# Kernel tuning notes

Hardware: AMD Instinct MI355X
Metric: run time of the kernel (lower is better)

## Reference

```python
import jax, jax.numpy as jnp
import numpy as np

B, KPLUS1, D = 64, 513, 1024

def setup_inputs() -> dict:
    key = jax.random.key(0)
    k1, k2, k3 = jax.random.split(key, 3)
    x = jax.random.normal(k1, (B, KPLUS1, D), dtype=jnp.float32)
    # glorot-style scaled init for faithfulness in magnitude
    dense_weights = jax.random.normal(k2, (2 * D, D), dtype=jnp.float32) * (1.0 / np.sqrt(2 * D))
    dot_bias = jax.random.normal(k3, (D, 1), dtype=jnp.float32) * (1.0 / np.sqrt(D))
    return {"x": x, "dense_weights": dense_weights, "dot_bias": dot_bias}

def reference(x, dense_weights, dot_bias):
    # x: [B, K+1, D]; x[:,0] = sentence encoding u, x[:,1:] = knowledge z_t
    u = x[:, 0, :]            # [B, D]
    z = x[:, 1:, :]           # [B, K, D]
    d = z.shape[-1]
    # concat(z_t, u) @ W1 == z @ W1[:D] + u @ W1[D:], broadcast over K
    # (mathematically identical to the tile+concat+matmul in the original)
    w_z = dense_weights[:d, :]   # [D, D]
    w_u = dense_weights[d:, :]   # [D, D]
    m = jnp.tanh(jnp.einsum('bkd,de->bke', z, w_z)
                 + jnp.einsum('bd,de->be', u, w_u)[:, None, :])  # [B, K, D]
    q = jnp.einsum('bke,e->bk', m, dot_bias[:, 0])               # [B, K]
    return jax.nn.softmax(q, axis=-1)                            # [B, K]
```

## Files before the change

### kernel.cpp

```cpp
#include <hip/hip_runtime.h>
#include <hip/hip_bf16.h>


typedef __attribute__((ext_vector_type(8))) short short8;
typedef __attribute__((ext_vector_type(8))) _Float16 half8;
typedef __attribute__((ext_vector_type(4))) float f32x4;
typedef unsigned short ushort_t;

typedef const __attribute__((address_space(1))) void gvoid_t;
typedef __attribute__((address_space(3))) void lvoid_t;

__device__ __forceinline__ ushort_t f2bf(float f) {
    unsigned u = __float_as_uint(f);
    unsigned r = u + 0x7FFFu + ((u >> 16) & 1u);
    return (ushort_t)(r >> 16);
}
__device__ __forceinline__ float bf2f(ushort_t h) {
    return __uint_as_float(((unsigned)h) << 16);
}
__device__ __forceinline__ float tanh_fast(float x) {
    float e = __expf(2.f * x);
    return 1.f - 2.f / (e + 1.f);
}

__global__ __launch_bounds__(256) void k_prep_z16(const float* __restrict__ x,
                                                  _Float16* __restrict__ z_h) {
    const int N8 = 32768 * 128;
    const int stride = 2048 * 256;
    for (int u = blockIdx.x * 256 + threadIdx.x; u < N8; u += stride) {
        const int m = u >> 7;
        const int c = (u & 127) * 8;
        const int b = m >> 9, k = m & 511;
        const float* src = x + ((size_t)(b * 513 + 1 + k) << 10) + c;
        const float4 v0 = *(const float4*)src;
        const float4 v1 = *(const float4*)(src + 4);
        half8 hv;
        hv[0] = (_Float16)v0.x; hv[1] = (_Float16)v0.y;
        hv[2] = (_Float16)v0.z; hv[3] = (_Float16)v0.w;
        hv[4] = (_Float16)v1.x; hv[5] = (_Float16)v1.y;
        hv[6] = (_Float16)v1.z; hv[7] = (_Float16)v1.w;
        *(half8*)(z_h + (size_t)m * 1024 + c) = hv;
    }
}

__global__ void k_prep_w16(const float* __restrict__ w,
                           _Float16* __restrict__ wzt) {
    __shared__ _Float16 th[64][66];
    const int k0 = blockIdx.x * 64;
    const int n0 = blockIdx.y * 64;
    const int t = threadIdx.x;
    const int lr = t >> 6;
    const int lc = t & 63;
#pragma unroll
    for (int r = 0; r < 16; ++r) {
        int kk = r * 4 + lr;
        th[kk][lc] = (_Float16)w[(size_t)(k0 + kk) * 1024 + n0 + lc];
    }
    __syncthreads();
#pragma unroll
    for (int r = 0; r < 16; ++r) {
        int nn = r * 4 + lr;
        wzt[(size_t)(n0 + nn) * 1024 + k0 + lc] = th[lc][nn];
    }
}

__global__ void k_hu(const float* __restrict__ x,
                     const float* __restrict__ w,
                     float* __restrict__ hu) {
    __shared__ float us[1024];
    const int b = blockIdx.y;
    const int e = blockIdx.x * 256 + threadIdx.x;
    for (int i = threadIdx.x; i < 1024; i += 256)
        us[i] = x[(size_t)b * 513 * 1024 + i];
    __syncthreads();
    const float* wu = w + (size_t)1024 * 1024;
    float acc = 0.f;
#pragma unroll 8
    for (int d = 0; d < 1024; ++d)
        acc = fmaf(us[d], wu[(size_t)d * 1024 + e], acc);
    hu[b * 1024 + e] = acc;
}

__global__ __launch_bounds__(256, 2) void k_gemm12(
        const _Float16* __restrict__ z_h,
        const _Float16* __restrict__ wzt,
        const float* __restrict__ hu,
        const float* __restrict__ bias,
        float* __restrict__ qp) {
    __shared__ __align__(16) _Float16 lds[3 * 12288];
    __shared__ float qred[2][2][128];

    const int t = threadIdx.x;
    const int mtile = blockIdx.x;
    const int ntile = blockIdx.y;
    const int wid = t >> 6;
    const int l = t & 63;
    const int wm = wid >> 1;
    const int wn = wid & 1;
    const int lr = l & 15;
    const int g = l >> 4;

    char* ldsb = (char*)lds;

    const int swz = (g ^ ((lr >> 1) & 3)) * 16;
    const int aOffRd = (wm * 128 + lr) * 64 + swz;
    const int bOffRd = (wn * 64 + lr) * 64 + swz;

    const int srow = t >> 2;
    const int schunk = ((t & 3) ^ ((t >> 3) & 3)) * 8;
    size_t aSrc[4], bSrc[2];
#pragma unroll
    for (int s = 0; s < 4; ++s)
        aSrc[s] = (size_t)(mtile * 256 + s * 64 + srow) * 1024 + schunk;
#pragma unroll
    for (int s = 0; s < 2; ++s)
        bSrc[s] = (size_t)(ntile * 128 + s * 64 + srow) * 1024 + schunk;

#define STAGE(kt, SLOT)                                                      \
    {   const int _kc = (kt) * 32;                                           \
        char* _d = ldsb + (SLOT) * 24576;                                    \
        _Pragma("unroll")                                                    \
        for (int s = 0; s < 4; ++s)                                          \
            __builtin_amdgcn_global_load_lds((gvoid_t*)(z_h + aSrc[s] + _kc),\
                (lvoid_t*)(_d + s * 4096 + t * 16), 16, 0, 0);               \
        _Pragma("unroll")                                                    \
        for (int s = 0; s < 2; ++s)                                          \
            __builtin_amdgcn_global_load_lds((gvoid_t*)(wzt + bSrc[s] + _kc),\
                (lvoid_t*)(_d + 16384 + s * 4096 + t * 16), 16, 0, 0); }

#define KBODY(T, SLOT, DOSTAGE, VMSTR)                                       \
    {   char* _sb = ldsb + (SLOT) * 24576;                                   \
        half8 afr[8], bfr[4];                                                \
        _Pragma("unroll")                                                    \
        for (int ni = 0; ni < 4; ++ni)                                       \
            bfr[ni] = *(const half8*)(_sb + 16384 + bOffRd + ni * 1024);     \
        _Pragma("unroll")                                                    \
        for (int mi = 0; mi < 8; ++mi)                                       \
            afr[mi] = *(const half8*)(_sb + aOffRd + mi * 1024);             \
        if (DOSTAGE) { STAGE((T) + 2, ((SLOT) + 2) % 3); }                   \
        asm volatile("s_waitcnt lgkmcnt(0)" ::: "memory");                   \
        __builtin_amdgcn_sched_barrier(0);                                   \
        __builtin_amdgcn_s_setprio(1);                                       \
        _Pragma("unroll")                                                    \
        for (int mi = 0; mi < 8; ++mi)                                       \
            _Pragma("unroll")                                                \
            for (int ni = 0; ni < 4; ++ni)                                   \
                acc[mi][ni] = __builtin_amdgcn_mfma_f32_16x16x32_f16(        \
                    afr[mi], bfr[ni], acc[mi][ni], 0, 0, 0);                 \
        __builtin_amdgcn_s_setprio(0);                                       \
        asm volatile(VMSTR ::: "memory");                                    \
        __builtin_amdgcn_sched_barrier(0);                                   \
        __builtin_amdgcn_s_barrier(); }

    f32x4 acc[8][4] = {};

    STAGE(0, 0); STAGE(1, 1);
    asm volatile("s_waitcnt vmcnt(6)" ::: "memory");
    __builtin_amdgcn_sched_barrier(0);
    __builtin_amdgcn_s_barrier();

#pragma unroll 1
    for (int i = 0; i < 10; ++i) {
        const int T = i * 3;
        KBODY(T + 0, 0, true, "s_waitcnt vmcnt(6)");
        KBODY(T + 1, 1, true, "s_waitcnt vmcnt(6)");
        KBODY(T + 2, 2, true, "s_waitcnt vmcnt(6)");
    }
    KBODY(30, 0, false, "s_waitcnt vmcnt(0)");
    KBODY(31, 1, false, "s_nop 0");
#undef KBODY
#undef STAGE

    const int lg = l >> 4;
    const int bb = mtile >> 1;
    float hu4[4], bias4[4];
#pragma unroll
    for (int ni = 0; ni < 4; ++ni) {
        int e = ntile * 128 + wn * 64 + ni * 16 + lr;
        hu4[ni] = hu[bb * 1024 + e];
        bias4[ni] = bias[e];
    }
#pragma unroll
    for (int mi = 0; mi < 8; ++mi) {
#pragma unroll
        for (int j = 0; j < 4; ++j) {
            float v = 0.f;
#pragma unroll
            for (int ni = 0; ni < 4; ++ni)
                v += tanh_fast(acc[mi][ni][j] + hu4[ni]) * bias4[ni];
            v += __shfl_xor(v, 1);
            v += __shfl_xor(v, 2);
            v += __shfl_xor(v, 4);
            v += __shfl_xor(v, 8);
            if (lr == 0)
                qred[wm][wn][mi * 16 + lg * 4 + j] = v;
        }
    }
    __syncthreads();
    if (t < 256) {
        float q = qred[t >> 7][0][t & 127] + qred[t >> 7][1][t & 127];
        qp[(size_t)ntile * 32768 + mtile * 256 + t] = q;
    }
}

__global__ void k_prep_w(const float* __restrict__ w,
                         ushort_t* __restrict__ wzt_hi,
                         ushort_t* __restrict__ wzt_lo) {
    __shared__ ushort_t th[64][66];
    __shared__ ushort_t tl[64][66];
    const int k0 = blockIdx.x * 64;
    const int n0 = blockIdx.y * 64;
    const int t = threadIdx.x;
    const int lr = t >> 6;
    const int lc = t & 63;
#pragma unroll
    for (int r = 0; r < 16; ++r) {
        int kk = r * 4 + lr;
        float f = w[(size_t)(k0 + kk) * 1024 + n0 + lc];
        ushort_t hi = f2bf(f);
        ushort_t lo = f2bf(f - bf2f(hi));
        th[kk][lc] = hi;
        tl[kk][lc] = lo;
    }
    __syncthreads();
#pragma unroll
    for (int r = 0; r < 16; ++r) {
        int nn = r * 4 + lr;
        wzt_hi[(size_t)(n0 + nn) * 1024 + k0 + lc] = th[lc][nn];
        wzt_lo[(size_t)(n0 + nn) * 1024 + k0 + lc] = tl[lc][nn];
    }
}

__global__ __launch_bounds__(256) void k_gemm(
        const float* __restrict__ x,
        const ushort_t* __restrict__ wzt_hi,
        const ushort_t* __restrict__ wzt_lo,
        const float* __restrict__ hu,
        const float* __restrict__ bias,
        float* __restrict__ qp) {
    __shared__ ushort_t As_hi[128][40];
    __shared__ ushort_t As_lo[128][40];
    __shared__ ushort_t Bs_hi[128][40];
    __shared__ ushort_t Bs_lo[128][40];
    __shared__ float qred[2][2][64];

    const int t = threadIdx.x;
    const int mtile = blockIdx.x;
    const int ntile = blockIdx.y;
    const int wid = t >> 6;
    const int l = t & 63;
    const int wm = wid >> 1;
    const int wn = wid & 1;

    f32x4 acc[4][4] = {};

    const int arow = t >> 3;
    const int acol = (t & 7) * 4;
    size_t abase[4];
#pragma unroll
    for (int it = 0; it < 4; ++it) {
        int m = mtile * 128 + arow + it * 32;
        int bb = m >> 9;
        int kk = m & 511;
        abase[it] = ((size_t)(bb * 513 + 1 + kk)) * 1024 + acol;
    }
    const int brow = t >> 2;
    const int bcol = (t & 3) * 8;
    const size_t bbase = (size_t)(ntile * 128 + brow) * 1024 + bcol;

    for (int k0 = 0; k0 < 1024; k0 += 32) {
#pragma unroll
        for (int it = 0; it < 4; ++it) {
            const float4 v = *(const float4*)(x + abase[it] + k0);
            ushort4 hv, lv;
            hv.x = f2bf(v.x); lv.x = f2bf(v.x - bf2f(hv.x));
            hv.y = f2bf(v.y); lv.y = f2bf(v.y - bf2f(hv.y));
            hv.z = f2bf(v.z); lv.z = f2bf(v.z - bf2f(hv.z));
            hv.w = f2bf(v.w); lv.w = f2bf(v.w - bf2f(hv.w));
            const int row = arow + it * 32;
            *(ushort4*)&As_hi[row][acol] = hv;
            *(ushort4*)&As_lo[row][acol] = lv;
        }
#pragma unroll
        for (int it = 0; it < 2; ++it) {
            const int row = brow + it * 64;
            const uint4 vh = *(const uint4*)(wzt_hi + bbase + (size_t)it * 64 * 1024 + k0);
            const uint4 vl = *(const uint4*)(wzt_lo + bbase + (size_t)it * 64 * 1024 + k0);
            *(uint4*)&Bs_hi[row][bcol] = vh;
            *(uint4*)&Bs_lo[row][bcol] = vl;
        }
        __syncthreads();

        const int lr = l & 15;
        const int lk = (l >> 4) * 8;
        short8 ah[4], al[4], bh[4], bl[4];
#pragma unroll
        for (int i = 0; i < 4; ++i) {
            ah[i] = *(const short8*)&As_hi[wm * 64 + i * 16 + lr][lk];
            al[i] = *(const short8*)&As_lo[wm * 64 + i * 16 + lr][lk];
            bh[i] = *(const short8*)&Bs_hi[wn * 64 + i * 16 + lr][lk];
            bl[i] = *(const short8*)&Bs_lo[wn * 64 + i * 16 + lr][lk];
        }
#pragma unroll
        for (int mi = 0; mi < 4; ++mi)
#pragma unroll
            for (int ni = 0; ni < 4; ++ni) {
                acc[mi][ni] = __builtin_amdgcn_mfma_f32_16x16x32_bf16(ah[mi], bh[ni], acc[mi][ni], 0, 0, 0);
                acc[mi][ni] = __builtin_amdgcn_mfma_f32_16x16x32_bf16(ah[mi], bl[ni], acc[mi][ni], 0, 0, 0);
                acc[mi][ni] = __builtin_amdgcn_mfma_f32_16x16x32_bf16(al[mi], bh[ni], acc[mi][ni], 0, 0, 0);
            }
        __syncthreads();
    }

    const int lr = l & 15;
    const int lg = l >> 4;
    const int bbatch = mtile >> 2;
    float hu4[4], bias4[4];
#pragma unroll
    for (int ni = 0; ni < 4; ++ni) {
        int e = ntile * 128 + wn * 64 + ni * 16 + lr;
        hu4[ni] = hu[bbatch * 1024 + e];
        bias4[ni] = bias[e];
    }
#pragma unroll
    for (int mi = 0; mi < 4; ++mi) {
#pragma unroll
        for (int j = 0; j < 4; ++j) {
            float v = 0.f;
#pragma unroll
            for (int ni = 0; ni < 4; ++ni)
                v += tanhf(acc[mi][ni][j] + hu4[ni]) * bias4[ni];
            v += __shfl_xor(v, 1);
            v += __shfl_xor(v, 2);
            v += __shfl_xor(v, 4);
            v += __shfl_xor(v, 8);
            if (lr == 0)
                qred[wm][wn][mi * 16 + lg * 4 + j] = v;
        }
    }
    __syncthreads();
    if (t < 128) {
        const int wmr = t >> 6;
        const int rr = t & 63;
        float qv = qred[wmr][0][rr] + qred[wmr][1][rr];
        qp[(size_t)ntile * 32768 + mtile * 128 + t] = qv;
    }
}

__global__ void k_softmax(const float* __restrict__ qp, float* __restrict__ out,
                          int nt) {
    const int b = blockIdx.x;
    const int k = threadIdx.x;
    float q = 0.f;
    for (int i = 0; i < nt; ++i)
        q += qp[(size_t)i * 32768 + b * 512 + k];

    __shared__ float redm[8];
    __shared__ float reds[8];
    const int wid = k >> 6;

    float m = q;
#pragma unroll
    for (int off = 32; off >= 1; off >>= 1)
        m = fmaxf(m, __shfl_xor(m, off));
    if ((k & 63) == 0) redm[wid] = m;
    __syncthreads();
    m = redm[0];
#pragma unroll
    for (int i = 1; i < 8; ++i) m = fmaxf(m, redm[i]);

    float p = expf(q - m);
    float s = p;
#pragma unroll
    for (int off = 32; off >= 1; off >>= 1)
        s += __shfl_xor(s, off);
    if ((k & 63) == 0) reds[wid] = s;
    __syncthreads();
    s = 0.f;
#pragma unroll
    for (int i = 0; i < 8; ++i) s += reds[i];

    out[b * 512 + k] = p / s;
}

extern "C" void kernel_launch(void* const* d_in, const int* in_sizes, int n_in,
                              void* d_out, int out_size, void* d_ws, size_t ws_size,
                              hipStream_t stream) {
    const float* x    = (const float*)d_in[0];
    const float* w    = (const float*)d_in[1];
    const float* bias = (const float*)d_in[2];
    float* out = (float*)d_out;

    char* ws = (char*)d_ws;
    const size_t ZN = (size_t)32768 * 1024;

    const size_t need = ZN * sizeof(_Float16)
                      + (size_t)1024 * 1024 * sizeof(_Float16)
                      + (size_t)64 * 1024 * sizeof(float)
                      + (size_t)8 * 32768 * sizeof(float);

    if (ws_size >= need) {
        _Float16* z_h = (_Float16*)ws;
        _Float16* wzt = z_h + ZN;
        float*    hu  = (float*)(wzt + (size_t)1024 * 1024);
        float*    qp  = hu + (size_t)64 * 1024;

        k_prep_z16<<<2048, 256, 0, stream>>>(x, z_h);
        k_prep_w16<<<dim3(16, 16), 256, 0, stream>>>(w, wzt);
        k_hu<<<dim3(4, 64), 256, 0, stream>>>(x, w, hu);
        k_gemm12<<<dim3(128, 8), 256, 0, stream>>>(z_h, wzt, hu, bias, qp);
        k_softmax<<<64, 512, 0, stream>>>(qp, out, 8);
    } else {
        ushort_t* wzt_hi = (ushort_t*)ws;
        ushort_t* wzt_lo = wzt_hi + (size_t)1024 * 1024;
        float* hu = (float*)(ws + (size_t)4 * 1024 * 1024);
        float* qp = hu + (size_t)64 * 1024;

        k_prep_w<<<dim3(16, 16), 256, 0, stream>>>(w, wzt_hi, wzt_lo);
        k_hu<<<dim3(4, 64), 256, 0, stream>>>(x, w, hu);
        k_gemm<<<dim3(256, 8), 256, 0, stream>>>(x, wzt_hi, wzt_lo, hu, bias, qp);
        k_softmax<<<64, 512, 0, stream>>>(qp, out, 8);
    }
}
```

Baseline: 185.2 us.

## Enlarge GEMM block tile to 256x256 with eight waves per block

The fused GEMM+tanh+dot kernel now uses 512-thread blocks, each computing a 256x256 output tile instead of 256x128. The grid is halved along N and the softmax reduces over four partial-q slices instead of eight. The goal is to cut global and L2 traffic per FLOP by reusing each A tile across twice as many columns. In exchange LDS use rises to 96KB per block and occupancy drops to roughly one block per CU.

```diff
diff --git a/kernel.cpp b/kernel.cpp
--- a/kernel.cpp
+++ b/kernel.cpp
@@ -81,22 +81,22 @@
     hu[b * 1024 + e] = acc;
 }
 
-__global__ __launch_bounds__(256, 2) void k_gemm12(
+__global__ __launch_bounds__(512) void k_gemm13(
         const _Float16* __restrict__ z_h,
         const _Float16* __restrict__ wzt,
         const float* __restrict__ hu,
         const float* __restrict__ bias,
         float* __restrict__ qp) {
-    __shared__ __align__(16) _Float16 lds[3 * 12288];
-    __shared__ float qred[2][2][128];
+    __shared__ __align__(16) _Float16 lds[3 * 16384];
+    __shared__ float qred[2][4][128];
 
     const int t = threadIdx.x;
     const int mtile = blockIdx.x;
     const int ntile = blockIdx.y;
     const int wid = t >> 6;
     const int l = t & 63;
-    const int wm = wid >> 1;
-    const int wn = wid & 1;
+    const int wm = wid >> 2;
+    const int wn = wid & 3;
     const int lr = l & 15;
     const int g = l >> 4;
 
@@ -104,36 +104,34 @@
 
     const int swz = (g ^ ((lr >> 1) & 3)) * 16;
     const int aOffRd = (wm * 128 + lr) * 64 + swz;
-    const int bOffRd = (wn * 64 + lr) * 64 + swz;
-
-    const int srow = t >> 2;
+    const int bOffRd = 16384 + (wn * 64 + lr) * 64 + swz;
+
     const int schunk = ((t & 3) ^ ((t >> 3) & 3)) * 8;
-    size_t aSrc[4], bSrc[2];
-#pragma unroll
-    for (int s = 0; s < 4; ++s)
-        aSrc[s] = (size_t)(mtile * 256 + s * 64 + srow) * 1024 + schunk;
-#pragma unroll
-    for (int s = 0; s < 2; ++s)
-        bSrc[s] = (size_t)(ntile * 128 + s * 64 + srow) * 1024 + schunk;
+    size_t aSrc[2], bSrc[2];
+#pragma unroll
+    for (int j = 0; j < 2; ++j) {
+        aSrc[j] = (size_t)(mtile * 256 + (t >> 2) + j * 128) * 1024 + schunk;
+        bSrc[j] = (size_t)(ntile * 256 + (t >> 2) + j * 128) * 1024 + schunk;
+    }
 
 #define STAGE(kt, SLOT)                                                      \
     {   const int _kc = (kt) * 32;                                           \
-        char* _d = ldsb + (SLOT) * 24576;                                    \
+        char* _d = ldsb + (SLOT) * 32768;                                    \
         _Pragma("unroll")                                                    \
-        for (int s = 0; s < 4; ++s)                                          \
-            __builtin_amdgcn_global_load_lds((gvoid_t*)(z_h + aSrc[s] + _kc),\
-                (lvoid_t*)(_d + s * 4096 + t * 16), 16, 0, 0);               \
+        for (int j = 0; j < 2; ++j)                                          \
+            __builtin_amdgcn_global_load_lds((gvoid_t*)(z_h + aSrc[j] + _kc),\
+                (lvoid_t*)(_d + t * 16 + j * 8192), 16, 0, 0);               \
         _Pragma("unroll")                                                    \
-        for (int s = 0; s < 2; ++s)                                          \
-            __builtin_amdgcn_global_load_lds((gvoid_t*)(wzt + bSrc[s] + _kc),\
-                (lvoid_t*)(_d + 16384 + s * 4096 + t * 16), 16, 0, 0); }
+        for (int j = 0; j < 2; ++j)                                          \
+            __builtin_amdgcn_global_load_lds((gvoid_t*)(wzt + bSrc[j] + _kc),\
+                (lvoid_t*)(_d + 16384 + t * 16 + j * 8192), 16, 0, 0); }
 
 #define KBODY(T, SLOT, DOSTAGE, VMSTR)                                       \
-    {   char* _sb = ldsb + (SLOT) * 24576;                                   \
+    {   char* _sb = ldsb + (SLOT) * 32768;                                   \
         half8 afr[8], bfr[4];                                                \
         _Pragma("unroll")                                                    \
         for (int ni = 0; ni < 4; ++ni)                                       \
-            bfr[ni] = *(const half8*)(_sb + 16384 + bOffRd + ni * 1024);     \
+            bfr[ni] = *(const half8*)(_sb + bOffRd + ni * 1024);             \
         _Pragma("unroll")                                                    \
         for (int mi = 0; mi < 8; ++mi)                                       \
             afr[mi] = *(const half8*)(_sb + aOffRd + mi * 1024);             \
@@ -155,28 +153,27 @@
     f32x4 acc[8][4] = {};
 
     STAGE(0, 0); STAGE(1, 1);
-    asm volatile("s_waitcnt vmcnt(6)" ::: "memory");
+    asm volatile("s_waitcnt vmcnt(4)" ::: "memory");
     __builtin_amdgcn_sched_barrier(0);
     __builtin_amdgcn_s_barrier();
 
 #pragma unroll 1
     for (int i = 0; i < 10; ++i) {
         const int T = i * 3;
-        KBODY(T + 0, 0, true, "s_waitcnt vmcnt(6)");
-        KBODY(T + 1, 1, true, "s_waitcnt vmcnt(6)");
-        KBODY(T + 2, 2, true, "s_waitcnt vmcnt(6)");
+        KBODY(T + 0, 0, true, "s_waitcnt vmcnt(4)");
+        KBODY(T + 1, 1, true, "s_waitcnt vmcnt(4)");
+        KBODY(T + 2, 2, true, "s_waitcnt vmcnt(4)");
     }
     KBODY(30, 0, false, "s_waitcnt vmcnt(0)");
     KBODY(31, 1, false, "s_nop 0");
 #undef KBODY
 #undef STAGE
 
-    const int lg = l >> 4;
     const int bb = mtile >> 1;
     float hu4[4], bias4[4];
 #pragma unroll
     for (int ni = 0; ni < 4; ++ni) {
-        int e = ntile * 128 + wn * 64 + ni * 16 + lr;
+        int e = ntile * 256 + wn * 64 + ni * 16 + lr;
         hu4[ni] = hu[bb * 1024 + e];
         bias4[ni] = bias[e];
     }
@@ -193,12 +190,15 @@
             v += __shfl_xor(v, 4);
             v += __shfl_xor(v, 8);
             if (lr == 0)
-                qred[wm][wn][mi * 16 + lg * 4 + j] = v;
+                qred[wm][wn][mi * 16 + g * 4 + j] = v;
         }
     }
     __syncthreads();
     if (t < 256) {
-        float q = qred[t >> 7][0][t & 127] + qred[t >> 7][1][t & 127];
+        const int wmr = t >> 7;
+        const int rr = t & 127;
+        float q = qred[wmr][0][rr] + qred[wmr][1][rr]
+                + qred[wmr][2][rr] + qred[wmr][3][rr];
         qp[(size_t)ntile * 32768 + mtile * 256 + t] = q;
     }
 }
@@ -397,7 +397,7 @@
     const size_t need = ZN * sizeof(_Float16)
                       + (size_t)1024 * 1024 * sizeof(_Float16)
                       + (size_t)64 * 1024 * sizeof(float)
-                      + (size_t)8 * 32768 * sizeof(float);
+                      + (size_t)4 * 32768 * sizeof(float);
 
     if (ws_size >= need) {
         _Float16* z_h = (_Float16*)ws;
@@ -408,8 +408,8 @@
         k_prep_z16<<<2048, 256, 0, stream>>>(x, z_h);
         k_prep_w16<<<dim3(16, 16), 256, 0, stream>>>(w, wzt);
         k_hu<<<dim3(4, 64), 256, 0, stream>>>(x, w, hu);
-        k_gemm12<<<dim3(128, 8), 256, 0, stream>>>(z_h, wzt, hu, bias, qp);
-        k_softmax<<<64, 512, 0, stream>>>(qp, out, 8);
+        k_gemm13<<<dim3(128, 4), 512, 0, stream>>>(z_h, wzt, hu, bias, qp);
+        k_softmax<<<64, 512, 0, stream>>>(qp, out, 4);
     } else {
         ushort_t* wzt_hi = (ushort_t*)ws;
         ushort_t* wzt_lo = wzt_hi + (size_t)1024 * 1024;
```

Measured after the change: 180.8 us. 2.3% less time.
